# Kernel optimization log

Measured on AMD Instinct MI355X. Metric: run time of the kernel, lower is better.

The kernel has to match this reference:

```python
import jax, jax.numpy as jnp
import numpy as np

N, NU, R, NX, NY = 8192, 4, 128, 64, 4


def setup_inputs() -> dict:
    key = jax.random.key(0)
    k1, k2, k3, k4, k5 = jax.random.split(key, 5)
    u = jax.random.normal(k1, (N, NU, R), dtype=jnp.float32)
    # Stable A: orthogonal matrix scaled to spectral radius 0.95 so the
    # 8192-step linear recurrence does not blow up numerically.
    A_raw = np.asarray(jax.random.normal(k2, (NX, NX), dtype=jnp.float32))
    Q, _ = np.linalg.qr(A_raw)
    A = jnp.asarray(0.95 * Q, dtype=jnp.float32)
    B_u = 0.1 * jax.random.normal(k3, (NX, NU), dtype=jnp.float32)
    C_y = 0.1 * jax.random.normal(k4, (NY, NX), dtype=jnp.float32)
    D_yu = 0.1 * jax.random.normal(k5, (NY, NU), dtype=jnp.float32)
    return {"u": u, "A": A, "B_u": B_u, "C_y": C_y, "D_yu": D_yu}


def reference(u, A, B_u, C_y, D_yu):
    """ModelBLA.simulate with handicap=0.

    u: (N, nu, R). Returns (Y, X) with Y: (N, ny, R), X: (N, nx, R).
    Recurrence (X_0 = 0):
        Y_k     = C_y @ X_k + D_yu @ U_k
        X_{k+1} = A   @ X_k + B_u  @ U_k
    X_k (pre-update state) is recorded at step k, matching the original.
    """
    nx = A.shape[0]
    r = u.shape[2]

    def step(X, U):  # X: (nx, R), U: (nu, R)
        Y = C_y @ X + D_yu @ U          # (ny, R)
        X_next = A @ X + B_u @ U        # (nx, R)
        return X_next, (Y, X)

    X0 = jnp.zeros((nx, r), dtype=u.dtype)
    _, (Y, X) = jax.lax.scan(step, X0, u)
    return Y, X
```

## Files before the change

### kernel.cpp

```cpp
#include <hip/hip_runtime.h>
#include <cstddef>


typedef unsigned short u16;
typedef unsigned int u32;
typedef __bf16 bf16x8 __attribute__((ext_vector_type(8)));
typedef float f32x4 __attribute__((ext_vector_type(4)));

#define NT 8192
#define RC 128
#define LCH 16
#define CCH 512
#define NMT 9
#define GW 72
#define NSEG 32
#define SEGL 16

#define OFF_POWS 0
#define OFF_Q    69632
#define OFF_R    73984
#define OFF_CQ   78336
#define OFF_KHF  78608
#define OFF_TOT  82704
#define B_MH  1379392
#define B_ML  1387584
#define B_KHH 1395776
#define B_KHL 1403968
#define B_WH  1412160
#define B_WL  1707072
#define OFF_V0 500496

#define SWZ_K(r,k) (((((k) >> 3) ^ ((r) & 7)) << 3) | ((k) & 7))

static __device__ __forceinline__ u16 f2bf(float v) {
  union { float f; u32 u; } x; x.f = v;
  u32 r = x.u + 0x7fffu + ((x.u >> 16) & 1u);
  return (u16)(r >> 16);
}
static __device__ __forceinline__ float bf2f(u16 h) {
  union { float f; u32 u; } x; x.u = ((u32)h) << 16; return x.f;
}
static __device__ __forceinline__ void split_bf(float v, u16& h, u16& l) {
  h = f2bf(v);
  l = f2bf(v - bf2f(h));
}

__global__ __launch_bounds__(256) void k_pow_init(const float* __restrict__ A,
                                                  float* __restrict__ ws)
{
  float* P = ws + OFF_POWS;
  int e = blockIdx.x * 256 + threadIdx.x;
  if (e < 4096) {
    P[e] = ((e >> 6) == (e & 63)) ? 1.f : 0.f;
    P[4096 + e] = A[e];
  }
}

__global__ __launch_bounds__(256) void k_pow_stage(float* __restrict__ ws, int base)
{
  __shared__ float sL[64 * 65], sR[64 * 65];
  float* P = ws + OFF_POWS;
  const int x = blockIdx.x;
  const float* L  = P + (size_t)base * 4096;
  const float* Rm = P + (size_t)(x + 1) * 4096;
  float* O        = P + (size_t)(base + 1 + x) * 4096;
  const int tid = threadIdx.x;
  for (int e = tid; e < 4096; e += 256) {
    sL[(e >> 6) * 65 + (e & 63)] = L[e];
    sR[(e >> 6) * 65 + (e & 63)] = Rm[e];
  }
  __syncthreads();
  const int it = tid >> 4, jt = tid & 15;
  float acc[4][4] = {};
  for (int k = 0; k < 64; k++) {
    float a[4], b[4];
    #pragma unroll
    for (int ii = 0; ii < 4; ii++) a[ii] = sL[(it * 4 + ii) * 65 + k];
    #pragma unroll
    for (int jj = 0; jj < 4; jj++) b[jj] = sR[k * 65 + jt * 4 + jj];
    #pragma unroll
    for (int ii = 0; ii < 4; ii++)
      #pragma unroll
      for (int jj = 0; jj < 4; jj++) acc[ii][jj] += a[ii] * b[jj];
  }
  #pragma unroll
  for (int ii = 0; ii < 4; ii++)
    #pragma unroll
    for (int jj = 0; jj < 4; jj++)
      O[(it * 4 + ii) * 64 + jt * 4 + jj] = acc[ii][jj];
}

__global__ __launch_bounds__(256) void k_tables(const float* __restrict__ Bu,
                                                const float* __restrict__ Cy,
                                                float* __restrict__ ws)
{
  __shared__ float sQ[256];
  float* P  = ws + OFF_POWS;
  float* Q  = ws + OFF_Q;
  float* R  = ws + OFF_R;
  float* CQ = ws + OFF_CQ;
  float* Kf = ws + OFF_KHF;
  const int d = blockIdx.x;
  const int tid = threadIdx.x;
  const float* Pd = P + (size_t)d * 4096;

  {
    int i = tid >> 2, ch = tid & 3;
    float acc = 0.f;
    for (int k = 0; k < 64; k++) acc += Pd[i * 64 + k] * Bu[k * 4 + ch];
    Q[d * 256 + tid] = acc;
    sQ[tid] = acc;
    if (d < 16) Kf[i * 64 + 4 * (15 - d) + ch] = acc;
  }
  {
    int y = tid >> 6, j = tid & 63;
    float acc = 0.f;
    for (int k = 0; k < 64; k++) acc += Cy[y * 64 + k] * Pd[k * 64 + j];
    R[d * 256 + y * 64 + j] = acc;
  }
  __syncthreads();
  if (tid < 16) {
    int y = tid >> 2, ch = tid & 3;
    float acc = 0.f;
    for (int k = 0; k < 64; k++) acc += Cy[y * 64 + k] * sQ[k * 4 + ch];
    CQ[d * 16 + y * 4 + ch] = acc;
  }
}

__global__ __launch_bounds__(256) void k_wbuild(float* __restrict__ ws,
                                                const float* __restrict__ Dyu)
{
  const float* P  = ws + OFF_POWS;
  const float* Q  = ws + OFF_Q;
  const float* R  = ws + OFF_R;
  const float* CQ = ws + OFF_CQ;
  const float* Kf = ws + OFF_KHF;
  u16* Wh  = (u16*)((char*)ws + B_WH);
  u16* Wl  = (u16*)((char*)ws + B_WL);
  u16* KhH = (u16*)((char*)ws + B_KHH);
  u16* KhL = (u16*)((char*)ws + B_KHL);
  u16* MhB = (u16*)((char*)ws + B_MH);
  u16* MlB = (u16*)((char*)ws + B_ML);

  int idx = blockIdx.x * 256 + threadIdx.x;
  if (idx < 1152 * 128) {
    int m = idx >> 7, kk = idx & 127;
    int t = m / GW, i = m - t * GW;
    float v = 0.f;
    if (i < 68) {
      if (kk < 64) {
        v = (i < 64) ? P[(size_t)t * 4096 + i * 64 + kk]
                     : R[t * 256 + (i - 64) * 64 + kk];
      } else {
        int tau = (kk - 64) >> 2, ch = (kk - 64) & 3;
        if (tau < t)
          v = (i < 64) ? Q[(t - 1 - tau) * 256 + i * 4 + ch]
                       : CQ[(t - 1 - tau) * 16 + (i - 64) * 4 + ch];
        else if (tau == t && i >= 64)
          v = Dyu[(i - 64) * 4 + ch];
      }
    }
    u16 h, l; split_bf(v, h, l);
    int off = m * 128 + (kk & 64) + SWZ_K(m, kk & 63);
    Wh[off] = h; Wl[off] = l;
  } else if (idx < 1152 * 128 + 4096) {
    int e = idx - 1152 * 128, i = e >> 6, k = e & 63;
    u16 h, l; split_bf(Kf[e], h, l);
    KhH[i * 64 + SWZ_K(i, k)] = h;
    KhL[i * 64 + SWZ_K(i, k)] = l;
  } else if (idx < 1152 * 128 + 8192) {
    int e = idx - 1152 * 128 - 4096, i = e >> 6, k = e & 63;
    u16 h, l; split_bf(P[16 * 4096 + e], h, l);
    MhB[i * 64 + SWZ_K(i, k)] = h;
    MlB[i * 64 + SWZ_K(i, k)] = l;
  }
}

__device__ void mfma_apply64(const u16* __restrict__ MhG, const u16* __restrict__ MlG,
                             const float* __restrict__ X, const float* __restrict__ addsrc,
                             float* __restrict__ out)
{
  __shared__ __align__(16) u16 sMh[4096], sMl[4096];
  __shared__ __align__(16) u16 sXh[8192], sXl[8192];
  const int tid = threadIdx.x;
  for (int e = tid; e < 2048; e += 256) {
    ((u32*)sMh)[e] = ((const u32*)MhG)[e];
    ((u32*)sMl)[e] = ((const u32*)MlG)[e];
  }
  for (int it = 0; it < 16; it++) {
    int idx = it * 256 + tid;
    int n = idx & 127, kk = (idx >> 7) * 2;
    float f0 = X[(size_t)kk * 128 + n];
    float f1 = X[(size_t)(kk + 1) * 128 + n];
    u16 h0, l0, h1, l1;
    split_bf(f0, h0, l0); split_bf(f1, h1, l1);
    int off = n * 64 + SWZ_K(n, kk);
    *(u32*)&sXh[off] = (u32)h0 | ((u32)h1 << 16);
    *(u32*)&sXl[off] = (u32)l0 | ((u32)l1 << 16);
  }
  __syncthreads();

  const int w = tid >> 6, lane = tid & 63, m16 = lane & 15, q = lane >> 4;
  f32x4 zero = {0.f, 0.f, 0.f, 0.f};
  f32x4 acc[4][2];
  for (int a = 0; a < 4; a++) for (int b = 0; b < 2; b++) acc[a][b] = zero;

  for (int prod = 0; prod < 3; prod++) {
    const u16* As = (prod == 2) ? sMl : sMh;
    const u16* Bs = (prod == 1) ? sXl : sXh;
    #pragma unroll
    for (int ks = 0; ks < 2; ks++) {
      const int kg = ks * 4 + q;
      bf16x8 bfr[2];
      #pragma unroll
      for (int fn = 0; fn < 2; fn++) {
        int n = w * 32 + fn * 16 + m16;
        bfr[fn] = *(const bf16x8*)&Bs[n * 64 + ((kg ^ (n & 7)) << 3)];
      }
      #pragma unroll
      for (int fm = 0; fm < 4; fm++) {
        int r = fm * 16 + m16;
        bf16x8 afr = *(const bf16x8*)&As[r * 64 + ((kg ^ (r & 7)) << 3)];
        #pragma unroll
        for (int fn = 0; fn < 2; fn++)
          acc[fm][fn] = __builtin_amdgcn_mfma_f32_16x16x32_bf16(afr, bfr[fn], acc[fm][fn], 0, 0, 0);
      }
    }
  }
  #pragma unroll
  for (int fm = 0; fm < 4; fm++)
    #pragma unroll
    for (int fn = 0; fn < 2; fn++)
      #pragma unroll
      for (int rg = 0; rg < 4; rg++) {
        int row = fm * 16 + q * 4 + rg;
        int col = w * 32 + fn * 16 + m16;
        float v = acc[fm][fn][rg];
        if (addsrc) v += addsrc[(size_t)row * 128 + col];
        out[(size_t)row * 128 + col] = v;
      }
}

__global__ __launch_bounds__(256) void k_contrib(const float* __restrict__ u,
                                                 const u16* __restrict__ KhH,
                                                 const u16* __restrict__ KhL,
                                                 float* __restrict__ V0)
{
  int b = blockIdx.x;
  mfma_apply64(KhH, KhL, u + (size_t)b * 8192, nullptr, V0 + (size_t)b * 8192);
}

__global__ __launch_bounds__(256) void k_scanseg(float* __restrict__ V,
                                                 float* __restrict__ Tot,
                                                 const u16* __restrict__ Mh,
                                                 const u16* __restrict__ Ml,
                                                 int mode)
{
  __shared__ __align__(16) u16 sMh[4096], sMl[4096];
  __shared__ __align__(16) u16 sZh[8192], sZl[8192];
  const int s = blockIdx.x;
  const int tid = threadIdx.x;

  for (int e = tid; e < 2048; e += 256) {
    ((u32*)sMh)[e] = ((const u32*)Mh)[e];
    ((u32*)sMl)[e] = ((const u32*)Ml)[e];
  }
  if (mode == 0 || s == 0) {
    for (int e = tid; e < 4096; e += 256) { ((u32*)sZh)[e] = 0u; ((u32*)sZl)[e] = 0u; }
  } else {
    const float* T = Tot + (size_t)(s - 1) * 8192;
    for (int it = 0; it < 16; it++) {
      int idx = it * 256 + tid;
      int n = idx & 127, kk = (idx >> 7) * 2;
      float f0 = T[(size_t)kk * 128 + n];
      float f1 = T[(size_t)(kk + 1) * 128 + n];
      u16 h0, l0, h1, l1;
      split_bf(f0, h0, l0); split_bf(f1, h1, l1);
      int off = n * 64 + SWZ_K(n, kk);
      *(u32*)&sZh[off] = (u32)h0 | ((u32)h1 << 16);
      *(u32*)&sZl[off] = (u32)l0 | ((u32)l1 << 16);
    }
  }
  __syncthreads();

  const int w = tid >> 6, lane = tid & 63, m16 = lane & 15, q = lane >> 4;
  const float* Vs = V + (size_t)s * SEGL * 8192;
  float wreg[32];
  #pragma unroll
  for (int fm = 0; fm < 4; fm++)
    #pragma unroll
    for (int fn = 0; fn < 2; fn++)
      #pragma unroll
      for (int rg = 0; rg < 4; rg++)
        wreg[fm * 8 + fn * 4 + rg] =
            Vs[(size_t)(fm * 16 + q * 4 + rg) * 128 + (w * 32 + fn * 16 + m16)];

  for (int t = 0; t < SEGL; t++) {
    f32x4 acc[4][2];
    #pragma unroll
    for (int fm = 0; fm < 4; fm++)
      #pragma unroll
      for (int fn = 0; fn < 2; fn++)
        #pragma unroll
        for (int rg = 0; rg < 4; rg++)
          acc[fm][fn][rg] = wreg[fm * 8 + fn * 4 + rg];
    if (t < SEGL - 1) {
      const float* Wn = Vs + (size_t)(t + 1) * 8192;
      #pragma unroll
      for (int fm = 0; fm < 4; fm++)
        #pragma unroll
        for (int fn = 0; fn < 2; fn++)
          #pragma unroll
          for (int rg = 0; rg < 4; rg++)
            wreg[fm * 8 + fn * 4 + rg] =
                Wn[(size_t)(fm * 16 + q * 4 + rg) * 128 + (w * 32 + fn * 16 + m16)];
    }
    for (int prod = 0; prod < 3; prod++) {
      const u16* As = (prod == 2) ? sMl : sMh;
      const u16* Bs = (prod == 1) ? sZl : sZh;
      #pragma unroll
      for (int ks = 0; ks < 2; ks++) {
        const int kg = ks * 4 + q;
        bf16x8 bfr[2];
        #pragma unroll
        for (int fn = 0; fn < 2; fn++) {
          int n = w * 32 + fn * 16 + m16;
          bfr[fn] = *(const bf16x8*)&Bs[n * 64 + ((kg ^ (n & 7)) << 3)];
        }
        #pragma unroll
        for (int fm = 0; fm < 4; fm++) {
          int r = fm * 16 + m16;
          bf16x8 afr = *(const bf16x8*)&As[r * 64 + ((kg ^ (r & 7)) << 3)];
          #pragma unroll
          for (int fn = 0; fn < 2; fn++)
            acc[fm][fn] = __builtin_amdgcn_mfma_f32_16x16x32_bf16(afr, bfr[fn], acc[fm][fn], 0, 0, 0);
        }
      }
    }
    __syncthreads();
    #pragma unroll
    for (int fm = 0; fm < 4; fm++)
      #pragma unroll
      for (int fn = 0; fn < 2; fn++) {
        int n = w * 32 + fn * 16 + m16;
        int k0 = fm * 16 + q * 4;
        u16 hh[4], ll[4];
        #pragma unroll
        for (int rg = 0; rg < 4; rg++) split_bf(acc[fm][fn][rg], hh[rg], ll[rg]);
        int off = n * 64 + SWZ_K(n, k0);
        *(u32*)&sZh[off]     = (u32)hh[0] | ((u32)hh[1] << 16);
        *(u32*)&sZh[off + 2] = (u32)hh[2] | ((u32)hh[3] << 16);
        *(u32*)&sZl[off]     = (u32)ll[0] | ((u32)ll[1] << 16);
        *(u32*)&sZl[off + 2] = (u32)ll[2] | ((u32)ll[3] << 16);
      }
    __syncthreads();
    if (mode == 1) {
      u16* dst = (u16*)(Vs + (size_t)t * 8192);
      for (int e = tid; e < 1024; e += 256) {
        ((uint4*)dst)[e]        = ((const uint4*)sZh)[e];
        ((uint4*)dst)[1024 + e] = ((const uint4*)sZl)[e];
      }
    } else if (t == SEGL - 1) {
      float* T = Tot + (size_t)s * 8192;
      #pragma unroll
      for (int fm = 0; fm < 4; fm++)
        #pragma unroll
        for (int fn = 0; fn < 2; fn++)
          #pragma unroll
          for (int rg = 0; rg < 4; rg++)
            T[(size_t)(fm * 16 + q * 4 + rg) * 128 + (w * 32 + fn * 16 + m16)] =
                acc[fm][fn][rg];
    }
  }
}

__global__ __launch_bounds__(256) void k_gemm(const float* __restrict__ u,
                                              const u16* __restrict__ Zt,
                                              const u16* __restrict__ Wh,
                                              const u16* __restrict__ Wl,
                                              float* __restrict__ Yout,
                                              float* __restrict__ Xout)
{
  __shared__ __align__(16) u16 sWh[8192], sWl[8192];
  __shared__ __align__(16) u16 sSh[8192], sSl[8192];
  const int bid0 = blockIdx.x;
  const int bid = (bid0 & 7) * (CCH * NMT / 8) + (bid0 >> 3);
  const int c = bid / NMT, mt = bid - c * NMT;
  const int tid = threadIdx.x;
  const int w = tid >> 6, lane = tid & 63, m16 = lane & 15, q = lane >> 4;
  const int wm = w >> 1, wn = w & 1;

  f32x4 zero = {0.f, 0.f, 0.f, 0.f};
  f32x4 acc[4][4];
  for (int a = 0; a < 4; a++) for (int b = 0; b < 4; b++) acc[a][b] = zero;

  for (int H = 0; H < 2; H++) {
    if (H) __syncthreads();
    for (int e = tid; e < 1024; e += 256) {
      int m_loc = e >> 3, seg = e & 7;
      size_t goff = (size_t)(mt * 128 + m_loc) * 128 + H * 64 + seg * 8;
      ((uint4*)sWh)[e] = *(const uint4*)(Wh + goff);
      ((uint4*)sWl)[e] = *(const uint4*)(Wl + goff);
    }
    if (H == 0) {
      if (c == 0) {
        uint4 z4 = {0u, 0u, 0u, 0u};
        for (int e = tid; e < 1024; e += 256) {
          ((uint4*)sSh)[e] = z4;
          ((uint4*)sSl)[e] = z4;
        }
      } else {
        const uint4* zt = (const uint4*)(Zt + (size_t)(c - 1) * 16384);
        for (int e = tid; e < 1024; e += 256) {
          ((uint4*)sSh)[e] = zt[e];
          ((uint4*)sSl)[e] = zt[1024 + e];
        }
      }
    } else {
      for (int it = 0; it < 16; it++) {
        int idx = it * 256 + tid;
        int n = idx & 127, k = (idx >> 7) * 2;
        float f0 = u[((size_t)c * 64 + k) * 128 + n];
        float f1 = u[((size_t)c * 64 + k + 1) * 128 + n];
        u16 h0, l0, h1, l1;
        split_bf(f0, h0, l0); split_bf(f1, h1, l1);
        int off = n * 64 + SWZ_K(n, k);
        *(u32*)&sSh[off] = (u32)h0 | ((u32)h1 << 16);
        *(u32*)&sSl[off] = (u32)l0 | ((u32)l1 << 16);
      }
    }
    __syncthreads();

    for (int prod = 0; prod < 3; prod++) {
      const u16* As = (prod == 2) ? sWl : sWh;
      const u16* Bs = (prod == 1) ? sSl : sSh;
      #pragma unroll
      for (int ks = 0; ks < 2; ks++) {
        const int kg = ks * 4 + q;
        bf16x8 bfr[4];
        #pragma unroll
        for (int fn = 0; fn < 4; fn++) {
          int n = wn * 64 + fn * 16 + m16;
          bfr[fn] = *(const bf16x8*)&Bs[n * 64 + ((kg ^ (n & 7)) << 3)];
        }
        #pragma unroll
        for (int fm = 0; fm < 4; fm++) {
          int r = wm * 64 + fm * 16 + m16;
          bf16x8 afr = *(const bf16x8*)&As[r * 64 + ((kg ^ (r & 7)) << 3)];
          #pragma unroll
          for (int fn = 0; fn < 4; fn++)
            acc[fm][fn] = __builtin_amdgcn_mfma_f32_16x16x32_bf16(afr, bfr[fn], acc[fm][fn], 0, 0, 0);
        }
      }
    }
  }
  #pragma unroll
  for (int fm = 0; fm < 4; fm++)
    #pragma unroll
    for (int fn = 0; fn < 4; fn++)
      #pragma unroll
      for (int rg = 0; rg < 4; rg++) {
        unsigned m_loc = wm * 64 + fm * 16 + q * 4 + rg;
        unsigned m = mt * 128 + m_loc;
        unsigned t = m / GW;
        unsigned i = m - t * GW;
        int col = wn * 64 + fn * 16 + m16;
        float v = acc[fm][fn][rg];
        size_t nt_ = (size_t)c * LCH + t;
        if (i < 64) Xout[(nt_ * 64 + i) * 128 + col] = v;
        else if (i < 68) Yout[(nt_ * 4 + (i - 64)) * 128 + col] = v;
      }
}

extern "C" void kernel_launch(void* const* d_in, const int* in_sizes, int n_in,
                              void* d_out, int out_size, void* d_ws, size_t ws_size,
                              hipStream_t stream)
{
  const float* u   = (const float*)d_in[0];
  const float* A   = (const float*)d_in[1];
  const float* Bu  = (const float*)d_in[2];
  const float* Cy  = (const float*)d_in[3];
  const float* Dyu = (const float*)d_in[4];
  float* ws = (float*)d_ws;
  float* Yout = (float*)d_out;
  float* Xout = Yout + (size_t)NT * 4 * RC;

  u16* MhB = (u16*)((char*)d_ws + B_MH);
  u16* MlB = (u16*)((char*)d_ws + B_ML);
  u16* KhH = (u16*)((char*)d_ws + B_KHH);
  u16* KhL = (u16*)((char*)d_ws + B_KHL);
  u16* Wh  = (u16*)((char*)d_ws + B_WH);
  u16* Wl  = (u16*)((char*)d_ws + B_WL);
  float* Tot = ws + OFF_TOT;
  float* V0  = ws + OFF_V0;

  hipLaunchKernelGGL(k_pow_init, dim3(16), dim3(256), 0, stream, A, ws);
  hipLaunchKernelGGL(k_pow_stage, dim3(1), dim3(256), 0, stream, ws, 1);
  hipLaunchKernelGGL(k_pow_stage, dim3(2), dim3(256), 0, stream, ws, 2);
  hipLaunchKernelGGL(k_pow_stage, dim3(4), dim3(256), 0, stream, ws, 4);
  hipLaunchKernelGGL(k_pow_stage, dim3(8), dim3(256), 0, stream, ws, 8);
  hipLaunchKernelGGL(k_tables, dim3(17), dim3(256), 0, stream, Bu, Cy, ws);
  hipLaunchKernelGGL(k_wbuild, dim3(608), dim3(256), 0, stream, ws, Dyu);
  hipLaunchKernelGGL(k_contrib, dim3(CCH), dim3(256), 0, stream, u, KhH, KhL, V0);
  hipLaunchKernelGGL(k_scanseg, dim3(NSEG), dim3(256), 0, stream, V0, Tot, MhB, MlB, 0);
  hipLaunchKernelGGL(k_scanseg, dim3(NSEG), dim3(256), 0, stream, V0, Tot, MhB, MlB, 1);
  hipLaunchKernelGGL(k_gemm, dim3(CCH * NMT), dim3(256), 0, stream,
                     u, (const u16*)V0, Wh, Wl, Yout, Xout);
}
```

Measured before the change: 467.3 us.

## Read GEMM weight and carry-state fragments directly from global memory instead of LDS

The output GEMM kernel no longer stages the W tiles and the carried-in state Z through shared memory. MFMA operand fragments for these are now loaded straight from global memory, which relies on the data already being stored in the swizzled layout and on L2 reuse across blocks. Only the split u tile still goes through LDS, and it is loaded once up front. This halves the LDS footprint per block and removes a barrier and a zero-fill. The zero-state products for the first chunk are now skipped entirely. The trade-off is more global and L2 traffic and higher latency on the A fragment loads, which LDS used to hide.

```diff
diff --git a/kernel.cpp b/kernel.cpp
--- a/kernel.cpp
+++ b/kernel.cpp
@@ -381,7 +381,6 @@
                                               float* __restrict__ Yout,
                                               float* __restrict__ Xout)
 {
-  __shared__ __align__(16) u16 sWh[8192], sWl[8192];
   __shared__ __align__(16) u16 sSh[8192], sSl[8192];
   const int bid0 = blockIdx.x;
   const int bid = (bid0 & 7) * (CCH * NMT / 8) + (bid0 >> 3);
@@ -390,50 +389,31 @@
   const int w = tid >> 6, lane = tid & 63, m16 = lane & 15, q = lane >> 4;
   const int wm = w >> 1, wn = w & 1;
 
+  for (int it = 0; it < 16; it++) {
+    int idx = it * 256 + tid;
+    int n = idx & 127, k = (idx >> 7) * 2;
+    float f0 = u[((size_t)c * 64 + k) * 128 + n];
+    float f1 = u[((size_t)c * 64 + k + 1) * 128 + n];
+    u16 h0, l0, h1, l1;
+    split_bf(f0, h0, l0); split_bf(f1, h1, l1);
+    int off = n * 64 + SWZ_K(n, k);
+    *(u32*)&sSh[off] = (u32)h0 | ((u32)h1 << 16);
+    *(u32*)&sSl[off] = (u32)l0 | ((u32)l1 << 16);
+  }
+
   f32x4 zero = {0.f, 0.f, 0.f, 0.f};
   f32x4 acc[4][4];
   for (int a = 0; a < 4; a++) for (int b = 0; b < 4; b++) acc[a][b] = zero;
 
-  for (int H = 0; H < 2; H++) {
-    if (H) __syncthreads();
-    for (int e = tid; e < 1024; e += 256) {
-      int m_loc = e >> 3, seg = e & 7;
-      size_t goff = (size_t)(mt * 128 + m_loc) * 128 + H * 64 + seg * 8;
-      ((uint4*)sWh)[e] = *(const uint4*)(Wh + goff);
-      ((uint4*)sWl)[e] = *(const uint4*)(Wl + goff);
-    }
-    if (H == 0) {
-      if (c == 0) {
-        uint4 z4 = {0u, 0u, 0u, 0u};
-        for (int e = tid; e < 1024; e += 256) {
-          ((uint4*)sSh)[e] = z4;
-          ((uint4*)sSl)[e] = z4;
-        }
-      } else {
-        const uint4* zt = (const uint4*)(Zt + (size_t)(c - 1) * 16384);
-        for (int e = tid; e < 1024; e += 256) {
-          ((uint4*)sSh)[e] = zt[e];
-          ((uint4*)sSl)[e] = zt[1024 + e];
-        }
-      }
-    } else {
-      for (int it = 0; it < 16; it++) {
-        int idx = it * 256 + tid;
-        int n = idx & 127, k = (idx >> 7) * 2;
-        float f0 = u[((size_t)c * 64 + k) * 128 + n];
-        float f1 = u[((size_t)c * 64 + k + 1) * 128 + n];
-        u16 h0, l0, h1, l1;
-        split_bf(f0, h0, l0); split_bf(f1, h1, l1);
-        int off = n * 64 + SWZ_K(n, k);
-        *(u32*)&sSh[off] = (u32)h0 | ((u32)h1 << 16);
-        *(u32*)&sSl[off] = (u32)l0 | ((u32)l1 << 16);
-      }
-    }
-    __syncthreads();
-
+  const u16* WhT = Wh + (size_t)mt * 128 * 128;
+  const u16* WlT = Wl + (size_t)mt * 128 * 128;
+
+  if (c > 0) {
+    const u16* ZhP = Zt + (size_t)(c - 1) * 16384;
+    const u16* ZlP = ZhP + 8192;
     for (int prod = 0; prod < 3; prod++) {
-      const u16* As = (prod == 2) ? sWl : sWh;
-      const u16* Bs = (prod == 1) ? sSl : sSh;
+      const u16* Ag = (prod == 2) ? WlT : WhT;
+      const u16* Bg = (prod == 1) ? ZlP : ZhP;
       #pragma unroll
       for (int ks = 0; ks < 2; ks++) {
         const int kg = ks * 4 + q;
@@ -441,12 +421,12 @@
         #pragma unroll
         for (int fn = 0; fn < 4; fn++) {
           int n = wn * 64 + fn * 16 + m16;
-          bfr[fn] = *(const bf16x8*)&Bs[n * 64 + ((kg ^ (n & 7)) << 3)];
+          bfr[fn] = *(const bf16x8*)&Bg[n * 64 + ((kg ^ (n & 7)) << 3)];
         }
         #pragma unroll
         for (int fm = 0; fm < 4; fm++) {
           int r = wm * 64 + fm * 16 + m16;
-          bf16x8 afr = *(const bf16x8*)&As[r * 64 + ((kg ^ (r & 7)) << 3)];
+          bf16x8 afr = *(const bf16x8*)&Ag[r * 128 + ((kg ^ (r & 7)) << 3)];
           #pragma unroll
           for (int fn = 0; fn < 4; fn++)
             acc[fm][fn] = __builtin_amdgcn_mfma_f32_16x16x32_bf16(afr, bfr[fn], acc[fm][fn], 0, 0, 0);
@@ -454,6 +434,31 @@
       }
     }
   }
+  __syncthreads();
+
+  for (int prod = 0; prod < 3; prod++) {
+    const u16* Ag = (prod == 2) ? WlT : WhT;
+    const u16* Bs = (prod == 1) ? sSl : sSh;
+    #pragma unroll
+    for (int ks = 0; ks < 2; ks++) {
+      const int kg = ks * 4 + q;
+      bf16x8 bfr[4];
+      #pragma unroll
+      for (int fn = 0; fn < 4; fn++) {
+        int n = wn * 64 + fn * 16 + m16;
+        bfr[fn] = *(const bf16x8*)&Bs[n * 64 + ((kg ^ (n & 7)) << 3)];
+      }
+      #pragma unroll
+      for (int fm = 0; fm < 4; fm++) {
+        int r = wm * 64 + fm * 16 + m16;
+        bf16x8 afr = *(const bf16x8*)&Ag[r * 128 + 64 + ((kg ^ (r & 7)) << 3)];
+        #pragma unroll
+        for (int fn = 0; fn < 4; fn++)
+          acc[fm][fn] = __builtin_amdgcn_mfma_f32_16x16x32_bf16(afr, bfr[fn], acc[fm][fn], 0, 0, 0);
+      }
+    }
+  }
+
   #pragma unroll
   for (int fm = 0; fm < 4; fm++)
     #pragma unroll
```

Result: no change. 463.7 us (-0.8%).

## Restructure k_gemm to one block per chunk looping over M tiles

Applied to the files above, without the earlier changes.

The final GEMM now launches one 512-thread block per time chunk instead of one block per (chunk, M-tile). The chunk's state and input operands are staged into shared memory once and reused across all nine M tiles. The W fragments are read directly from global memory, presumably served from cache, instead of being staged into LDS. The first chunk skips the zero-state half of the product. This removes the repeated staging of the B operand and the u split for every M tile, but it trades away LDS staging of W and cuts the grid to 512 blocks, which may reduce latency hiding.

```diff
diff --git a/kernel.cpp b/kernel.cpp
--- a/kernel.cpp
+++ b/kernel.cpp
@@ -374,102 +374,95 @@
   }
 }
 
-__global__ __launch_bounds__(256) void k_gemm(const float* __restrict__ u,
-                                              const u16* __restrict__ Zt,
-                                              const u16* __restrict__ Wh,
-                                              const u16* __restrict__ Wl,
-                                              float* __restrict__ Yout,
-                                              float* __restrict__ Xout)
-{
-  __shared__ __align__(16) u16 sWh[8192], sWl[8192];
-  __shared__ __align__(16) u16 sSh[8192], sSl[8192];
-  const int bid0 = blockIdx.x;
-  const int bid = (bid0 & 7) * (CCH * NMT / 8) + (bid0 >> 3);
-  const int c = bid / NMT, mt = bid - c * NMT;
+__global__ __launch_bounds__(512, 4) void k_gemm(const float* __restrict__ u,
+                                                 const u16* __restrict__ Zt,
+                                                 const u16* __restrict__ Wh,
+                                                 const u16* __restrict__ Wl,
+                                                 float* __restrict__ Yout,
+                                                 float* __restrict__ Xout)
+{
+  __shared__ __align__(16) u16 sSh[16384], sSl[16384];
+  const int c = blockIdx.x;
   const int tid = threadIdx.x;
   const int w = tid >> 6, lane = tid & 63, m16 = lane & 15, q = lane >> 4;
-  const int wm = w >> 1, wn = w & 1;
-
-  f32x4 zero = {0.f, 0.f, 0.f, 0.f};
-  f32x4 acc[4][4];
-  for (int a = 0; a < 4; a++) for (int b = 0; b < 4; b++) acc[a][b] = zero;
-
-  for (int H = 0; H < 2; H++) {
-    if (H) __syncthreads();
-    for (int e = tid; e < 1024; e += 256) {
-      int m_loc = e >> 3, seg = e & 7;
-      size_t goff = (size_t)(mt * 128 + m_loc) * 128 + H * 64 + seg * 8;
-      ((uint4*)sWh)[e] = *(const uint4*)(Wh + goff);
-      ((uint4*)sWl)[e] = *(const uint4*)(Wl + goff);
-    }
-    if (H == 0) {
-      if (c == 0) {
-        uint4 z4 = {0u, 0u, 0u, 0u};
-        for (int e = tid; e < 1024; e += 256) {
-          ((uint4*)sSh)[e] = z4;
-          ((uint4*)sSl)[e] = z4;
+  const int wm3 = w >> 1, wn = w & 1;
+
+  if (c == 0) {
+    uint4 z4 = {0u, 0u, 0u, 0u};
+    for (int e = tid; e < 1024; e += 512) {
+      ((uint4*)sSh)[e] = z4;
+      ((uint4*)sSl)[e] = z4;
+    }
+  } else {
+    const uint4* zt = (const uint4*)(Zt + (size_t)(c - 1) * 16384);
+    for (int e = tid; e < 1024; e += 512) {
+      ((uint4*)sSh)[e] = zt[e];
+      ((uint4*)sSl)[e] = zt[1024 + e];
+    }
+  }
+  for (int it = 0; it < 8; it++) {
+    int idx = it * 512 + tid;
+    int n = idx & 127, k = (idx >> 7) * 2;
+    float f0 = u[((size_t)c * 64 + k) * 128 + n];
+    float f1 = u[((size_t)c * 64 + k + 1) * 128 + n];
+    u16 h0, l0, h1, l1;
+    split_bf(f0, h0, l0); split_bf(f1, h1, l1);
+    int off = 8192 + n * 64 + SWZ_K(n, k);
+    *(u32*)&sSh[off] = (u32)h0 | ((u32)h1 << 16);
+    *(u32*)&sSl[off] = (u32)l0 | ((u32)l1 << 16);
+  }
+  __syncthreads();
+
+  for (int mt = 0; mt < NMT; mt++) {
+    const u16* WhT = Wh + (size_t)mt * 16384;
+    const u16* WlT = Wl + (size_t)mt * 16384;
+    f32x4 zero = {0.f, 0.f, 0.f, 0.f};
+    f32x4 acc[2][4];
+    for (int a = 0; a < 2; a++) for (int b = 0; b < 4; b++) acc[a][b] = zero;
+
+    #pragma unroll
+    for (int half = 0; half < 2; half++) {
+      if (half == 0 && c == 0) continue;
+      for (int prod = 0; prod < 3; prod++) {
+        const u16* Ag = (prod == 2) ? WlT : WhT;
+        const u16* Bs = (prod == 1) ? sSl : sSh;
+        #pragma unroll
+        for (int ks = 0; ks < 2; ks++) {
+          const int kg = ks * 4 + q;
+          bf16x8 bfr[4];
+          #pragma unroll
+          for (int fn = 0; fn < 4; fn++) {
+            int n = wn * 64 + fn * 16 + m16;
+            bfr[fn] = *(const bf16x8*)&Bs[half * 8192 + n * 64 + ((kg ^ (n & 7)) << 3)];
+          }
+          #pragma unroll
+          for (int fm = 0; fm < 2; fm++) {
+            int r = wm3 * 32 + fm * 16 + m16;
+            bf16x8 afr = *(const bf16x8*)&Ag[r * 128 + half * 64 + ((kg ^ (r & 7)) << 3)];
+            #pragma unroll
+            for (int fn = 0; fn < 4; fn++)
+              acc[fm][fn] = __builtin_amdgcn_mfma_f32_16x16x32_bf16(afr, bfr[fn], acc[fm][fn], 0, 0, 0);
+          }
         }
-      } else {
-        const uint4* zt = (const uint4*)(Zt + (size_t)(c - 1) * 16384);
-        for (int e = tid; e < 1024; e += 256) {
-          ((uint4*)sSh)[e] = zt[e];
-          ((uint4*)sSl)[e] = zt[1024 + e];
+      }
+    }
+    #pragma unroll
+    for (int fm = 0; fm < 2; fm++)
+      #pragma unroll
+      for (int fn = 0; fn < 4; fn++)
+        #pragma unroll
+        for (int rg = 0; rg < 4; rg++) {
+          unsigned m_loc = wm3 * 32 + fm * 16 + q * 4 + rg;
+          unsigned m = mt * 128 + m_loc;
+          unsigned t = m / GW;
+          unsigned i = m - t * GW;
+          int col = wn * 64 + fn * 16 + m16;
+          float v = acc[fm][fn][rg];
+          size_t nt_ = (size_t)c * LCH + t;
+          if (i < 64) Xout[(nt_ * 64 + i) * 128 + col] = v;
+          else if (i < 68) Yout[(nt_ * 4 + (i - 64)) * 128 + col] = v;
         }
-      }
-    } else {
-      for (int it = 0; it < 16; it++) {
-        int idx = it * 256 + tid;
-        int n = idx & 127, k = (idx >> 7) * 2;
-        float f0 = u[((size_t)c * 64 + k) * 128 + n];
-        float f1 = u[((size_t)c * 64 + k + 1) * 128 + n];
-        u16 h0, l0, h1, l1;
-        split_bf(f0, h0, l0); split_bf(f1, h1, l1);
-        int off = n * 64 + SWZ_K(n, k);
-        *(u32*)&sSh[off] = (u32)h0 | ((u32)h1 << 16);
-        *(u32*)&sSl[off] = (u32)l0 | ((u32)l1 << 16);
-      }
-    }
-    __syncthreads();
-
-    for (int prod = 0; prod < 3; prod++) {
-      const u16* As = (prod == 2) ? sWl : sWh;
-      const u16* Bs = (prod == 1) ? sSl : sSh;
-      #pragma unroll
-      for (int ks = 0; ks < 2; ks++) {
-        const int kg = ks * 4 + q;
-        bf16x8 bfr[4];
-        #pragma unroll
-        for (int fn = 0; fn < 4; fn++) {
-          int n = wn * 64 + fn * 16 + m16;
-          bfr[fn] = *(const bf16x8*)&Bs[n * 64 + ((kg ^ (n & 7)) << 3)];
-        }
-        #pragma unroll
-        for (int fm = 0; fm < 4; fm++) {
-          int r = wm * 64 + fm * 16 + m16;
-          bf16x8 afr = *(const bf16x8*)&As[r * 64 + ((kg ^ (r & 7)) << 3)];
-          #pragma unroll
-          for (int fn = 0; fn < 4; fn++)
-            acc[fm][fn] = __builtin_amdgcn_mfma_f32_16x16x32_bf16(afr, bfr[fn], acc[fm][fn], 0, 0, 0);
-        }
-      }
-    }
-  }
-  #pragma unroll
-  for (int fm = 0; fm < 4; fm++)
-    #pragma unroll
-    for (int fn = 0; fn < 4; fn++)
-      #pragma unroll
-      for (int rg = 0; rg < 4; rg++) {
-        unsigned m_loc = wm * 64 + fm * 16 + q * 4 + rg;
-        unsigned m = mt * 128 + m_loc;
-        unsigned t = m / GW;
-        unsigned i = m - t * GW;
-        int col = wn * 64 + fn * 16 + m16;
-        float v = acc[fm][fn][rg];
-        size_t nt_ = (size_t)c * LCH + t;
-        if (i < 64) Xout[(nt_ * 64 + i) * 128 + col] = v;
-        else if (i < 68) Yout[(nt_ * 4 + (i - 64)) * 128 + col] = v;
-      }
+  }
 }
 
 extern "C" void kernel_launch(void* const* d_in, const int* in_sizes, int n_in,
@@ -504,6 +497,6 @@
   hipLaunchKernelGGL(k_contrib, dim3(CCH), dim3(256), 0, stream, u, KhH, KhL, V0);
   hipLaunchKernelGGL(k_scanseg, dim3(NSEG), dim3(256), 0, stream, V0, Tot, MhB, MlB, 0);
   hipLaunchKernelGGL(k_scanseg, dim3(NSEG), dim3(256), 0, stream, V0, Tot, MhB, MlB, 1);
-  hipLaunchKernelGGL(k_gemm, dim3(CCH * NMT), dim3(256), 0, stream,
+  hipLaunchKernelGGL(k_gemm, dim3(CCH), dim3(512), 0, stream,
                      u, (const u16*)V0, Wh, Wl, Yout, Xout);
 }
```

Result: slower. 539.4 us (+15.4%).
